# Kernel tuning notes

Measured on AMD Instinct MI355X. Metric: run time of the kernel, lower is better.

Reference implementation:

```python
import jax, jax.numpy as jnp
import numpy as np
from jax import lax

N, D, A, R = 4096, 64, 8192, 8192
SCALE = 0.03
K_SAMP, K_ATT, K_REP = 6, 3, 10
# forward() default hyperparams; note the original passes (a_o, k_o) positionally
# into kernel(x, y, k, a), so k<-a_o and a<-k_o (all equal here anyway).
A_O = K_O = A_R = K_R = 0.1
A_ON = K_ON = A_RN = K_RN = 0.006


def _sqdist(x, y):
    # pairwise squared euclidean == l2_loss(x, y) with reduction='sum' per pair
    x2 = jnp.sum(x * x, axis=-1)[:, None]
    y2 = jnp.sum(y * y, axis=-1)[None, :]
    return jnp.maximum(x2 + y2 - 2.0 * (x @ y.T), 0.0)


def _rayleigh(dx, k, a):
    # k/a * dx * exp(-0.5*(dx/a)^2), dx is the summed squared distance
    return (k / a) * dx * jnp.exp(-0.5 * (dx / a) ** 2)


def _negexp(dx, k, a):
    # k * exp(-a * dx^2)
    return k * jnp.exp(-a * dx * dx)


def setup_inputs() -> dict:
    key = jax.random.key(0)
    k1, k2, k3 = jax.random.split(key, 3)
    return {
        "data": jax.random.normal(k1, (N, D), dtype=jnp.float32) * SCALE,
        "attracts": jax.random.normal(k2, (A, D), dtype=jnp.float32) * SCALE,
        "repels": jax.random.normal(k3, (R, D), dtype=jnp.float32) * SCALE,
        "epochs": 3,
    }


def reference(data, attracts, repels, epochs):
    """Vectorized (synchronous-update) supervised neural gas.

    Each epoch: every node finds its 5 nearest samples (edges, skipping the
    closest), its 3 nearest attracts and 10 nearest repels; it moves toward
    attracts (rayleigh kernel) and away from repels (neg-exp kernel). Each
    node additionally pushes its graph neighbors using its own nearest
    attracts (a_on/k_on) while neighbors are repelled with a_rn/k_rn.
    Updates are applied synchronously from pre-step vectors.
    """
    n = data.shape[0]
    src = jnp.repeat(jnp.arange(n), K_SAMP - 1)  # [E]

    def step(v, _):
        # edges: nearest samples in ORIGINAL data positions (self.data is never
        # updated inside forward), queried with current node vectors
        d_sd = _sqdist(v, data)                       # [N, N]
        _, nbr = lax.top_k(-d_sd, K_SAMP)
        tgt = nbr[:, 1:].reshape(-1)                  # [E] skip nearest

        # attract forces on the node itself
        d_sa = _sqdist(v, attracts)                   # [N, A]
        _, ia = lax.top_k(-d_sa, K_ATT)               # [N, 3]
        gk = attracts[ia]                             # [N, 3, D]
        dxa = jnp.take_along_axis(d_sa, ia, axis=1)   # [N, 3]
        e_o = _rayleigh(dxa, A_O, K_O)
        mv_a = jnp.einsum('nk,nkd->nd', e_o, gk - v[:, None])

        # repel forces on the node itself
        d_sr = _sqdist(v, repels)                     # [N, R]
        _, ir = lax.top_k(-d_sr, K_REP)               # [N, 10]
        rv = repels[ir]                               # [N, 10, D]
        dxr = jnp.take_along_axis(d_sr, ir, axis=1)
        e_r = _negexp(dxr, A_R, K_R)
        mv_r = jnp.einsum('nk,nkd->nd', e_r, rv - v[:, None])
        move_self = mv_a - mv_r

        # neighbor attract: source node's nearest attracts act on neighbor vectors
        g_e = gk[src]                                 # [E, 3, D]
        vj = v[tgt]                                   # [E, D]
        dx_on = jnp.sum((g_e - vj[:, None]) ** 2, axis=-1)  # [E, 3]
        e_on = _rayleigh(dx_on, A_ON, K_ON)
        mv_on = jnp.einsum('ek,ekd->ed', e_on, g_e - vj[:, None])
        nb_attr = jax.ops.segment_sum(mv_on, tgt, num_segments=n)

        # neighbor repel: each visited neighbor gets its own repel move (rn coeffs),
        # applied once per incoming edge
        e_rn = _negexp(dxr, A_RN, K_RN)
        mv_rn = jnp.einsum('nk,nkd->nd', e_rn, rv - v[:, None])
        indeg = jax.ops.segment_sum(jnp.ones_like(tgt, dtype=v.dtype), tgt,
                                    num_segments=n)
        nb_move = nb_attr - indeg[:, None] * mv_rn

        return v + move_self + nb_move, None

    v_final, _ = lax.scan(step, data, None, length=int(epochs))
    return v_final
```

## Files before the change

### kernel.cpp

```cpp
#include <hip/hip_runtime.h>
#include <math.h>

#define NN 4096
#define DD 64
#define NA 8192
#define NR 8192
#define NC (NN + NA + NR)
#define KS 6
#define KA 3
#define KR 10
#define EE (NN * (KS - 1))

#define CH 256
#define NCH0 (NN / CH)
#define NCH1 (NA / CH)
#define NCH2 (NR / CH)
#define NCHT (NCH0 + NCH1 + NCH2)
#define GROUPS (NN / 128)

typedef __attribute__((ext_vector_type(8))) short bf16x8;
typedef __attribute__((ext_vector_type(16))) float f32x16;
typedef unsigned long long u64;
#define MFMA32 __builtin_amdgcn_mfma_f32_32x32x16_bf16

__device__ __forceinline__ ushort f2bf(float f) {
    unsigned u = __float_as_uint(f);
    u += 0x7fffu + ((u >> 16) & 1u);
    return (ushort)(u >> 16);
}
__device__ __forceinline__ float bf2f(ushort b) {
    return __uint_as_float(((unsigned)b) << 16);
}
__device__ __forceinline__ u64 packdi(float d, int i) {
    return (((u64)__float_as_uint(d)) << 32) | (unsigned)i;
}
__device__ __forceinline__ float updist(u64 p) {
    return __uint_as_float((unsigned)(p >> 32));
}
__device__ __forceinline__ int upidx(u64 p) { return (int)(p & 0xffffffffu); }
__device__ __forceinline__ u64 umn64(u64 a, u64 b) { return a < b ? a : b; }
__device__ __forceinline__ u64 umx64(u64 a, u64 b) { return a > b ? a : b; }
__device__ __forceinline__ void cas64(u64& a, u64& b) {
    const bool s = b < a;
    const u64 mn = s ? b : a;
    const u64 mx = s ? a : b;
    a = mn;
    b = mx;
}

template <int N>
__device__ __forceinline__ void sortN(u64* S) {
#pragma unroll
    for (int p = 1; p < N; p <<= 1) {
#pragma unroll
        for (int k = p; k > 0; k >>= 1) {
#pragma unroll
            for (int j = k % p; j + k < N; j += 2 * k) {
#pragma unroll
                for (int i = 0; i < k; ++i) {
                    if (i + j + k < N &&
                        (i + j) / (2 * p) == (i + j + k) / (2 * p))
                        cas64(S[i + j], S[i + j + k]);
                }
            }
        }
    }
}

template <int K, int NA_, int NB_>
__device__ __forceinline__ void mergeTop(const u64* A, const u64* B, u64* R) {
#pragma unroll
    for (int k = 0; k < K; ++k) {
        u64 m = ~0ull;
        if (k < NA_) m = A[k];
        if (k < NB_) m = umn64(m, B[k]);
#pragma unroll
        for (int i = 0; i < k; ++i) {
            const int j = k - 1 - i;
            if (i < NA_ && j < NB_) m = umn64(m, umx64(A[i], B[j]));
        }
        R[k] = m;
    }
}

template <int K>
__device__ __forceinline__ void tileSelect(u64 (&bd)[K], u64 (&S)[16]) {
    u64 nb[K];
    if constexpr (K == 10) {
        sortN<16>(S);
        mergeTop<10, 10, 16>(bd, S, nb);
    } else if constexpr (K == 6) {
        sortN<8>(S);
        sortN<8>(S + 8);
        u64 t[6];
        mergeTop<6, 8, 8>(S, S + 8, t);
        mergeTop<6, 6, 6>(bd, t, nb);
    } else {
        sortN<4>(S);
        sortN<4>(S + 4);
        sortN<4>(S + 8);
        sortN<4>(S + 12);
        u64 t0[3], t1[3], t2[3];
        mergeTop<3, 4, 4>(S, S + 4, t0);
        mergeTop<3, 4, 4>(S + 8, S + 12, t1);
        mergeTop<3, 3, 3>(t0, t1, t2);
        mergeTop<3, 3, 3>(bd, t2, nb);
    }
#pragma unroll
    for (int k = 0; k < K; ++k) bd[k] = nb[k];
}

__global__ __launch_bounds__(256) void split_kernel(
    const float* __restrict__ x, int nrows, ushort* __restrict__ h,
    ushort* __restrict__ m, ushort* __restrict__ l, float* __restrict__ nrm) {
    const int idx = blockIdx.x * 256 + threadIdx.x;
    const int row = idx >> 6, lane = idx & 63;
    if (row >= nrows) return;
    const float xv = x[idx];
    const ushort hb = f2bf(xv);
    const float r1 = xv - bf2f(hb);
    const ushort mb = f2bf(r1);
    const float r2 = r1 - bf2f(mb);
    const ushort lb = f2bf(r2);
    h[idx] = hb;
    m[idx] = mb;
    l[idx] = lb;
    float sq = xv * xv;
#pragma unroll
    for (int off = 32; off > 0; off >>= 1) sq += __shfl_xor(sq, off, 64);
    if (lane == 0) nrm[row] = sq;
}

template <int K>
__device__ __forceinline__ void sweep_impl(
    const ushort* __restrict__ ch, const ushort* __restrict__ cm,
    const ushort* __restrict__ cl, const float* __restrict__ cnormp,
    const ushort* __restrict__ vh, const ushort* __restrict__ vm,
    const ushort* __restrict__ vl, const float* __restrict__ vnormp,
    u64* __restrict__ pp, int nchp, int up, int g) {
    const int tid = threadIdx.x, wave = tid >> 6, lane = tid & 63;
    const int n0 = g * 128 + wave * 32;
    const int node = n0 + (lane & 31);
    const int kq = (lane >> 5) * 8;

    const size_t vb = (size_t)node * DD + kq;
    bf16x8 bh[4], bm[4], bl[4];
#pragma unroll
    for (int m = 0; m < 4; ++m) {
        bh[m] = *(const bf16x8*)(vh + vb + 16 * m);
        bm[m] = *(const bf16x8*)(vm + vb + 16 * m);
        bl[m] = *(const bf16x8*)(vl + vb + 16 * m);
    }
    const float vn = vnormp[node];

    u64 bd[K];
#pragma unroll
    for (int k = 0; k < K; ++k) bd[k] = ~0ull;

    const int cbase = up * CH;
    const int rowA = lane & 31;
    const int r0 = (lane >> 5) * 4;

    for (int t = 0; t < CH / 32; ++t) {
        const int c0 = cbase + t * 32;
        const size_t ab = (size_t)(c0 + rowA) * DD + kq;
        bf16x8 ah[4], am[4], al[4];
#pragma unroll
        for (int m = 0; m < 4; ++m) {
            ah[m] = *(const bf16x8*)(ch + ab + 16 * m);
            am[m] = *(const bf16x8*)(cm + ab + 16 * m);
            al[m] = *(const bf16x8*)(cl + ab + 16 * m);
        }
        f32x16 acc = {0.f, 0.f, 0.f, 0.f, 0.f, 0.f, 0.f, 0.f,
                      0.f, 0.f, 0.f, 0.f, 0.f, 0.f, 0.f, 0.f};
#pragma unroll
        for (int m = 0; m < 4; ++m) {
            acc = MFMA32(ah[m], bl[m], acc, 0, 0, 0);
            acc = MFMA32(al[m], bh[m], acc, 0, 0, 0);
            acc = MFMA32(am[m], bm[m], acc, 0, 0, 0);
            acc = MFMA32(ah[m], bm[m], acc, 0, 0, 0);
            acc = MFMA32(am[m], bh[m], acc, 0, 0, 0);
            acc = MFMA32(ah[m], bh[m], acc, 0, 0, 0);
        }
        u64 S[16];
#pragma unroll
        for (int b = 0; b < 4; ++b) {
            const float4 cn = *(const float4*)(cnormp + c0 + r0 + 8 * b);
            const float cna[4] = {cn.x, cn.y, cn.z, cn.w};
#pragma unroll
            for (int a = 0; a < 4; ++a) {
                const float dist =
                    fmaxf(vn + cna[a] - 2.f * acc[b * 4 + a], 0.f);
                S[b * 4 + a] = packdi(dist, c0 + r0 + 8 * b + a);
            }
        }
        tileSelect<K>(bd, S);
    }
    u64 pb[K], od[K];
#pragma unroll
    for (int k = 0; k < K; ++k) pb[k] = __shfl_xor(bd[k], 32, 64);
    mergeTop<K, K, K>(bd, pb, od);
    if (lane < 32) {
        const int n = n0 + lane;
        const size_t base = ((size_t)n * nchp + up) * K;
#pragma unroll
        for (int k = 0; k < K; ++k) pp[base + k] = od[k];
    }
}

__global__ __launch_bounds__(256) void sweep_kernel(
    const ushort* __restrict__ ch, const ushort* __restrict__ cm,
    const ushort* __restrict__ cl, const float* __restrict__ cnorm,
    const ushort* __restrict__ vh, const ushort* __restrict__ vm,
    const ushort* __restrict__ vl, const float* __restrict__ vnorm,
    u64* __restrict__ pp) {
    const int g = blockIdx.x / NCHT;
    const int u = blockIdx.x % NCHT;
    const size_t o1 = (size_t)NN * DD, o2 = (size_t)(NN + NA) * DD;
    const size_t p1 = (size_t)NN * NCH0 * KS;
    const size_t p2 = p1 + (size_t)NN * NCH1 * KA;
    if (u < NCH0) {
        sweep_impl<KS>(ch, cm, cl, cnorm, vh, vm, vl, vnorm, pp, NCH0, u, g);
    } else if (u < NCH0 + NCH1) {
        sweep_impl<KA>(ch + o1, cm + o1, cl + o1, cnorm + NN, vh, vm, vl,
                       vnorm, pp + p1, NCH1, u - NCH0, g);
    } else {
        sweep_impl<KR>(ch + o2, cm + o2, cl + o2, cnorm + NN + NA, vh, vm, vl,
                       vnorm, pp + p2, NCH2, u - NCH0 - NCH1, g);
    }
}

template <int K, int NCH>
__device__ __forceinline__ void mergeN(const u64* __restrict__ pp, int n,
                                       u64* __restrict__ w, int lane) {
    __syncthreads();
    for (int j = lane; j < NCH * K; j += 64)
        w[j] = pp[(size_t)n * NCH * K + j];
    __syncthreads();
#pragma unroll
    for (int off = NCH / 2; off >= 1; off >>= 1) {
        if (lane < off) {
            const int a0 = lane * K, b0 = (lane + off) * K;
            u64 md[K];
            int p = 0, q = 0;
#pragma unroll
            for (int k = 0; k < K; ++k) {
                const u64 av = w[a0 + p];
                const u64 bv = w[b0 + q];
                const bool ta = av < bv;
                md[k] = ta ? av : bv;
                if (ta) ++p; else ++q;
            }
#pragma unroll
            for (int k = 0; k < K; ++k) w[a0 + k] = md[k];
        }
        __syncthreads();
    }
}

__global__ __launch_bounds__(256) void finalize_kernel(
    const float* __restrict__ v, const float* __restrict__ attr,
    const float* __restrict__ rep, const u64* __restrict__ pp,
    float* __restrict__ move_self, float* __restrict__ mv_rn,
    int* __restrict__ ia_out, int* __restrict__ tgt_out) {
    __shared__ u64 sp[4][NCH2 * KR];
    const int wave = threadIdx.x >> 6, lane = threadIdx.x & 63;
    const int n = blockIdx.x * 4 + wave;
    const float vv = v[n * DD + lane];
    const size_t p1 = (size_t)NN * NCH0 * KS;
    const size_t p2 = p1 + (size_t)NN * NCH1 * KA;

    mergeN<KS, NCH0>(pp, n, sp[wave], lane);
    if (lane < KS - 1) tgt_out[n * (KS - 1) + lane] = upidx(sp[wave][1 + lane]);

    mergeN<KA, NCH1>(pp + p1, n, sp[wave], lane);
    float mva = 0.f;
    if (lane < KA) ia_out[n * KA + lane] = upidx(sp[wave][lane]);
#pragma unroll
    for (int k = 0; k < KA; ++k) {
        const float dx = updist(sp[wave][k]);
        const int ik = upidx(sp[wave][k]);
        const float t = dx * 10.f;
        const float eo = dx * expf(-0.5f * t * t);
        mva = fmaf(eo, attr[(size_t)ik * DD + lane] - vv, mva);
    }

    mergeN<KR, NCH2>(pp + p2, n, sp[wave], lane);
    float mr = 0.f, mrn = 0.f;
#pragma unroll
    for (int k = 0; k < KR; ++k) {
        const float dx = updist(sp[wave][k]);
        const int ik = upidx(sp[wave][k]);
        const float er = 0.1f * expf(-0.1f * dx * dx);
        const float ern = 0.006f * expf(-0.006f * dx * dx);
        const float diff = rep[(size_t)ik * DD + lane] - vv;
        mr = fmaf(er, diff, mr);
        mrn = fmaf(ern, diff, mrn);
    }
    move_self[n * DD + lane] = mva - mr;
    mv_rn[n * DD + lane] = mrn;
}

__global__ __launch_bounds__(256) void edge_kernel(
    const float* __restrict__ v, const float* __restrict__ attr,
    const int* __restrict__ ia, const int* __restrict__ tgt,
    float* __restrict__ nb_attr, float* __restrict__ indeg) {
    const int lane = threadIdx.x & 63;
    const int w = threadIdx.x >> 6;
    const int e = blockIdx.x * 4 + w;
    if (e >= EE) return;
    const int s = e / (KS - 1);
    const int t = tgt[e];
    const float vj = v[t * DD + lane];
    float acc = 0.f;
#pragma unroll
    for (int k = 0; k < KA; ++k) {
        const int g = ia[s * KA + k];
        const float diff = attr[(size_t)g * DD + lane] - vj;
        float sq = diff * diff;
#pragma unroll
        for (int off = 32; off > 0; off >>= 1) sq += __shfl_xor(sq, off, 64);
        const float r = sq / 0.006f;
        const float eon = sq * expf(-0.5f * r * r);
        acc = fmaf(eon, diff, acc);
    }
    atomicAdd(&nb_attr[t * DD + lane], acc);
    if (lane == 0) atomicAdd(&indeg[t], 1.0f);
}

__global__ __launch_bounds__(256) void update_kernel(
    const float* __restrict__ v, const float* __restrict__ ms,
    const float* __restrict__ nba, const float* __restrict__ mrn,
    const float* __restrict__ indeg, float* __restrict__ vout) {
    const int i = blockIdx.x * 256 + threadIdx.x;
    if (i >= NN * DD) return;
    const int n = i >> 6;
    vout[i] = v[i] + ms[i] + nba[i] - indeg[n] * mrn[i];
}

extern "C" void kernel_launch(void* const* d_in, const int* in_sizes, int n_in,
                              void* d_out, int out_size, void* d_ws,
                              size_t ws_size, hipStream_t stream) {
    const float* data = (const float*)d_in[0];
    const float* attr = (const float*)d_in[1];
    const float* rep = (const float*)d_in[2];

    char* p = (char*)d_ws;
    auto alloc = [&](size_t bytes) {
        bytes = (bytes + 255) & ~(size_t)255;
        char* r = p;
        p += bytes;
        return (void*)r;
    };
    float* va = (float*)alloc(NN * DD * 4);
    float* vb = (float*)alloc(NN * DD * 4);
    float* ms = (float*)alloc(NN * DD * 4);
    float* mrn = (float*)alloc(NN * DD * 4);
    float* nba = (float*)alloc(NN * DD * 4 + NN * 4);
    float* indeg = nba + NN * DD;
    float* cnorm = (float*)alloc(NC * 4);
    float* vnorm = (float*)alloc(NN * 4);
    ushort* chv = (ushort*)alloc((size_t)NC * DD * 2);
    ushort* cmv = (ushort*)alloc((size_t)NC * DD * 2);
    ushort* clv = (ushort*)alloc((size_t)NC * DD * 2);
    ushort* vhb = (ushort*)alloc((size_t)NN * DD * 2);
    ushort* vmb = (ushort*)alloc((size_t)NN * DD * 2);
    ushort* vlb = (ushort*)alloc((size_t)NN * DD * 2);
    const size_t NPART =
        (size_t)NN * (NCH0 * KS + NCH1 * KA + NCH2 * KR);
    u64* pp = (u64*)alloc(NPART * 8);
    int* ia = (int*)alloc(NN * KA * 4);
    int* tgt = (int*)alloc(NN * (KS - 1) * 4);

    split_kernel<<<NN * DD / 256, 256, 0, stream>>>(data, NN, chv, cmv, clv,
                                                    cnorm);
    split_kernel<<<NA * DD / 256, 256, 0, stream>>>(
        attr, NA, chv + (size_t)NN * DD, cmv + (size_t)NN * DD,
        clv + (size_t)NN * DD, cnorm + NN);
    split_kernel<<<NR * DD / 256, 256, 0, stream>>>(
        rep, NR, chv + (size_t)(NN + NA) * DD, cmv + (size_t)(NN + NA) * DD,
        clv + (size_t)(NN + NA) * DD, cnorm + NN + NA);

    const float* vcur = data;
    float* outs[3] = {va, vb, (float*)d_out};
    for (int ep = 0; ep < 3; ++ep) {
        const ushort *evh, *evm, *evl;
        const float* evn;
        if (ep == 0) {
            evh = chv; evm = cmv; evl = clv; evn = cnorm;
        } else {
            split_kernel<<<NN * DD / 256, 256, 0, stream>>>(vcur, NN, vhb, vmb,
                                                            vlb, vnorm);
            evh = vhb; evm = vmb; evl = vlb; evn = vnorm;
        }
        sweep_kernel<<<GROUPS * NCHT, 256, 0, stream>>>(chv, cmv, clv, cnorm,
                                                        evh, evm, evl, evn, pp);
        finalize_kernel<<<NN / 4, 256, 0, stream>>>(vcur, attr, rep, pp, ms,
                                                    mrn, ia, tgt);
        hipMemsetAsync(nba, 0, (NN * DD + NN) * sizeof(float), stream);
        edge_kernel<<<(EE + 3) / 4, 256, 0, stream>>>(vcur, attr, ia, tgt, nba,
                                                      indeg);
        update_kernel<<<NN * DD / 256, 256, 0, stream>>>(vcur, ms, nba, mrn,
                                                         indeg, outs[ep]);
        vcur = outs[ep];
    }
}
```

Baseline: 627.9 us.

## Cut sweep register pressure: stream operands per k-step, select in 8-wide halves

The sweep kernel no longer keeps the node's hi/mid/lo bf16 fragments in registers for the whole loop. It reloads them together with the candidate fragments on each k-step of the MFMA loop. Top-k selection now runs on two 8-element halves per tile instead of one 16-element sort, and launch bounds request 8 blocks per multiprocessor. All three changes aim to lower VGPR usage and raise occupancy. The cost is redundant global or cache loads of node data on every tile, and possible spills or extra merge work under the tighter register cap.

```diff
diff --git a/kernel.cpp b/kernel.cpp
--- a/kernel.cpp
+++ b/kernel.cpp
@@ -40,16 +40,17 @@
 __device__ __forceinline__ int upidx(u64 p) { return (int)(p & 0xffffffffu); }
 __device__ __forceinline__ u64 umn64(u64 a, u64 b) { return a < b ? a : b; }
 __device__ __forceinline__ u64 umx64(u64 a, u64 b) { return a > b ? a : b; }
-__device__ __forceinline__ void cas64(u64& a, u64& b) {
-    const bool s = b < a;
-    const u64 mn = s ? b : a;
-    const u64 mx = s ? a : b;
+
+template <typename T>
+__device__ __forceinline__ void cas(T& a, T& b) {
+    const T mn = a < b ? a : b;
+    const T mx = a < b ? b : a;
     a = mn;
     b = mx;
 }
 
-template <int N>
-__device__ __forceinline__ void sortN(u64* S) {
+template <typename T, int N>
+__device__ __forceinline__ void sortN(T* S) {
 #pragma unroll
     for (int p = 1; p < N; p <<= 1) {
 #pragma unroll
@@ -60,7 +61,7 @@
                 for (int i = 0; i < k; ++i) {
                     if (i + j + k < N &&
                         (i + j) / (2 * p) == (i + j + k) / (2 * p))
-                        cas64(S[i + j], S[i + j + k]);
+                        cas(S[i + j], S[i + j + k]);
                 }
             }
         }
@@ -84,27 +85,17 @@
 }
 
 template <int K>
-__device__ __forceinline__ void tileSelect(u64 (&bd)[K], u64 (&S)[16]) {
+__device__ __forceinline__ void tileSelect8(u64 (&bd)[K], u64 (&S)[8]) {
     u64 nb[K];
-    if constexpr (K == 10) {
-        sortN<16>(S);
-        mergeTop<10, 10, 16>(bd, S, nb);
-    } else if constexpr (K == 6) {
-        sortN<8>(S);
-        sortN<8>(S + 8);
-        u64 t[6];
-        mergeTop<6, 8, 8>(S, S + 8, t);
-        mergeTop<6, 6, 6>(bd, t, nb);
+    if constexpr (K == 3) {
+        sortN<u64, 4>(S);
+        sortN<u64, 4>(S + 4);
+        u64 t0[3];
+        mergeTop<3, 4, 4>(S, S + 4, t0);
+        mergeTop<3, 3, 3>(bd, t0, nb);
     } else {
-        sortN<4>(S);
-        sortN<4>(S + 4);
-        sortN<4>(S + 8);
-        sortN<4>(S + 12);
-        u64 t0[3], t1[3], t2[3];
-        mergeTop<3, 4, 4>(S, S + 4, t0);
-        mergeTop<3, 4, 4>(S + 8, S + 12, t1);
-        mergeTop<3, 3, 3>(t0, t1, t2);
-        mergeTop<3, 3, 3>(bd, t2, nb);
+        sortN<u64, 8>(S);
+        mergeTop<K, K, 8>(bd, S, nb);
     }
 #pragma unroll
     for (int k = 0; k < K; ++k) bd[k] = nb[k];
@@ -143,15 +134,8 @@
     const int node = n0 + (lane & 31);
     const int kq = (lane >> 5) * 8;
 
-    const size_t vb = (size_t)node * DD + kq;
-    bf16x8 bh[4], bm[4], bl[4];
-#pragma unroll
-    for (int m = 0; m < 4; ++m) {
-        bh[m] = *(const bf16x8*)(vh + vb + 16 * m);
-        bm[m] = *(const bf16x8*)(vm + vb + 16 * m);
-        bl[m] = *(const bf16x8*)(vl + vb + 16 * m);
-    }
     const float vn = vnormp[node];
+    const size_t vOff = (size_t)node * DD + kq;
 
     u64 bd[K];
 #pragma unroll
@@ -163,38 +147,41 @@
 
     for (int t = 0; t < CH / 32; ++t) {
         const int c0 = cbase + t * 32;
-        const size_t ab = (size_t)(c0 + rowA) * DD + kq;
-        bf16x8 ah[4], am[4], al[4];
-#pragma unroll
-        for (int m = 0; m < 4; ++m) {
-            ah[m] = *(const bf16x8*)(ch + ab + 16 * m);
-            am[m] = *(const bf16x8*)(cm + ab + 16 * m);
-            al[m] = *(const bf16x8*)(cl + ab + 16 * m);
-        }
+        const size_t aOff = (size_t)(c0 + rowA) * DD + kq;
         f32x16 acc = {0.f, 0.f, 0.f, 0.f, 0.f, 0.f, 0.f, 0.f,
                       0.f, 0.f, 0.f, 0.f, 0.f, 0.f, 0.f, 0.f};
 #pragma unroll
         for (int m = 0; m < 4; ++m) {
-            acc = MFMA32(ah[m], bl[m], acc, 0, 0, 0);
-            acc = MFMA32(al[m], bh[m], acc, 0, 0, 0);
-            acc = MFMA32(am[m], bm[m], acc, 0, 0, 0);
-            acc = MFMA32(ah[m], bm[m], acc, 0, 0, 0);
-            acc = MFMA32(am[m], bh[m], acc, 0, 0, 0);
-            acc = MFMA32(ah[m], bh[m], acc, 0, 0, 0);
-        }
-        u64 S[16];
-#pragma unroll
-        for (int b = 0; b < 4; ++b) {
-            const float4 cn = *(const float4*)(cnormp + c0 + r0 + 8 * b);
-            const float cna[4] = {cn.x, cn.y, cn.z, cn.w};
-#pragma unroll
-            for (int a = 0; a < 4; ++a) {
-                const float dist =
-                    fmaxf(vn + cna[a] - 2.f * acc[b * 4 + a], 0.f);
-                S[b * 4 + a] = packdi(dist, c0 + r0 + 8 * b + a);
+            const bf16x8 Ah = *(const bf16x8*)(ch + aOff + 16 * m);
+            const bf16x8 Am = *(const bf16x8*)(cm + aOff + 16 * m);
+            const bf16x8 Al = *(const bf16x8*)(cl + aOff + 16 * m);
+            const bf16x8 Bh = *(const bf16x8*)(vh + vOff + 16 * m);
+            const bf16x8 Bm = *(const bf16x8*)(vm + vOff + 16 * m);
+            const bf16x8 Bl = *(const bf16x8*)(vl + vOff + 16 * m);
+            acc = MFMA32(Ah, Bl, acc, 0, 0, 0);
+            acc = MFMA32(Al, Bh, acc, 0, 0, 0);
+            acc = MFMA32(Am, Bm, acc, 0, 0, 0);
+            acc = MFMA32(Ah, Bm, acc, 0, 0, 0);
+            acc = MFMA32(Am, Bh, acc, 0, 0, 0);
+            acc = MFMA32(Ah, Bh, acc, 0, 0, 0);
+        }
+#pragma unroll
+        for (int p = 0; p < 2; ++p) {
+            u64 S[8];
+#pragma unroll
+            for (int b2 = 0; b2 < 2; ++b2) {
+                const int b = p * 2 + b2;
+                const float4 cn = *(const float4*)(cnormp + c0 + r0 + 8 * b);
+                const float cna[4] = {cn.x, cn.y, cn.z, cn.w};
+#pragma unroll
+                for (int a = 0; a < 4; ++a) {
+                    const float dist =
+                        fmaxf(vn + cna[a] - 2.f * acc[b * 4 + a], 0.f);
+                    S[b2 * 4 + a] = packdi(dist, c0 + r0 + 8 * b + a);
+                }
             }
-        }
-        tileSelect<K>(bd, S);
+            tileSelect8<K>(bd, S);
+        }
     }
     u64 pb[K], od[K];
 #pragma unroll
@@ -208,7 +195,7 @@
     }
 }
 
-__global__ __launch_bounds__(256) void sweep_kernel(
+__global__ __launch_bounds__(256, 8) void sweep_kernel(
     const ushort* __restrict__ ch, const ushort* __restrict__ cm,
     const ushort* __restrict__ cl, const float* __restrict__ cnorm,
     const ushort* __restrict__ vh, const ushort* __restrict__ vm,
```

New measurement: 1.065 ms. 1.7x slower.
